# Kernel optimization log

Measured on AMD Instinct MI355X. Metric: run time of the kernel, lower is better.

Reference implementation:

```python
import jax, jax.numpy as jnp
import numpy as np

N_NODES = 50000
N_EDGES = 600000
D_IN = 128
D_HID = 128


def _sage_conv(x, src, dst, W_l, b_l, W_r):
    """PyG SAGEConv (mean aggr): out = lin_l(mean_{j in N(i)} x_j) + lin_r(x_i).
    bias lives in lin_l only."""
    n = x.shape[0]
    agg = jax.ops.segment_sum(x[src], dst, num_segments=n)            # [N, D]
    cnt = jax.ops.segment_sum(jnp.ones((src.shape[0],), x.dtype), dst, num_segments=n)
    mean = agg / jnp.maximum(cnt, 1.0)[:, None]
    return mean @ W_l.T + b_l + x @ W_r.T


def setup_inputs() -> dict:
    key = jax.random.key(0)
    ks = jax.random.split(key, 8)
    glorot = lambda k, o, i: jax.random.normal(k, (o, i), jnp.float32) * np.sqrt(2.0 / (o + i))
    return {
        "x": jax.random.normal(ks[0], (N_NODES, D_IN), jnp.float32),
        "edge_index": jax.random.randint(ks[1], (2, N_EDGES), 0, N_NODES, jnp.int64),
        "W1_l": glorot(ks[2], D_HID, D_IN),
        "b1": jnp.zeros((D_HID,), jnp.float32),
        "W1_r": glorot(ks[3], D_HID, D_IN),
        "W2_l": glorot(ks[4], D_HID, D_HID),
        "b2": jnp.zeros((D_HID,), jnp.float32),
        "W2_r": glorot(ks[5], D_HID, D_HID),
    }


def reference(x, edge_index, W1_l, b1, W1_r, W2_l, b2, W2_r):
    src, dst = edge_index[0], edge_index[1]
    h = _sage_conv(x, src, dst, W1_l, b1, W1_r)
    h = jax.nn.leaky_relu(h, negative_slope=0.2)
    return _sage_conv(h, src, dst, W2_l, b2, W2_r)
```

## Files before the change

kernel.cpp:

```cpp
#include <hip/hip_runtime.h>

#define N_NODES 50000
#define N_EDGES 600000
#define D 128
#define SCAN_BLOCKS ((N_NODES + 255) / 256)

typedef __attribute__((ext_vector_type(8))) short bf16x8;
typedef __attribute__((ext_vector_type(4))) float floatx4;

__device__ inline unsigned int f2bf(float f) {
    unsigned int u = __float_as_uint(f);
    return (u + 0x7FFFu + ((u >> 16) & 1u)) >> 16;
}
__device__ inline float bf_lo(unsigned int u) { return __uint_as_float(u << 16); }
__device__ inline float bf_hi(unsigned int u) { return __uint_as_float(u & 0xFFFF0000u); }

__global__ void k_prep(const float* __restrict__ x, unsigned short* __restrict__ xbf,
                       const float* __restrict__ wa, const float* __restrict__ wb,
                       const float* __restrict__ wc, const float* __restrict__ wd,
                       unsigned short* __restrict__ wbf,
                       const int* __restrict__ dst, int* __restrict__ cnt) {
    const int b = blockIdx.x;
    const int t = threadIdx.x;
    if (b < 6250) {
        int i = b * 256 + t;
        float4 v = ((const float4*)x)[i];
        uint2 o;
        o.x = f2bf(v.x) | (f2bf(v.y) << 16);
        o.y = f2bf(v.z) | (f2bf(v.w) << 16);
        ((uint2*)xbf)[i] = o;
    } else if (b < 6506) {
        int i = (b - 6250) * 256 + t;
        const float* srcs[4] = {wa, wb, wc, wd};
        wbf[i] = (unsigned short)f2bf(srcs[i >> 14][i & 16383]);
    } else {
        int e = (b - 6506) * 256 + t;
        if (e < N_EDGES) atomicAdd(&cnt[dst[e]], 1);
    }
}


__global__ void k_scan1(const int* __restrict__ cnt, int* __restrict__ off,
                        int* __restrict__ partial) {
    __shared__ int sdata[256];
    const int t = threadIdx.x;
    const int i = blockIdx.x * 256 + t;
    int v = (i < N_NODES) ? cnt[i] : 0;
    sdata[t] = v;
    __syncthreads();
    for (int d = 1; d < 256; d <<= 1) {
        int u = (t >= d) ? sdata[t - d] : 0;
        __syncthreads();
        sdata[t] += u;
        __syncthreads();
    }
    if (i < N_NODES) off[i] = sdata[t] - v;
    if (t == 255) partial[blockIdx.x] = sdata[255];
}

__global__ void k_scan2(int* __restrict__ partial) {
    __shared__ int sdata[256];
    const int t = threadIdx.x;
    int v = (t < SCAN_BLOCKS) ? partial[t] : 0;
    sdata[t] = v;
    __syncthreads();
    for (int d = 1; d < 256; d <<= 1) {
        int u = (t >= d) ? sdata[t - d] : 0;
        __syncthreads();
        sdata[t] += u;
        __syncthreads();
    }
    if (t < SCAN_BLOCKS) partial[t] = sdata[t] - v;
}

__global__ void k_scan3(int* __restrict__ off, const int* __restrict__ partial,
                        int* __restrict__ cursor) {
    const int i = blockIdx.x * 256 + threadIdx.x;
    if (i < N_NODES) {
        int o = off[i] + partial[blockIdx.x];
        off[i] = o;
        cursor[i] = o;
    }
    if (i == 0) off[N_NODES] = N_EDGES;
}

__global__ void k_bucket(const int* __restrict__ src, const int* __restrict__ dst,
                         int* __restrict__ cursor, int* __restrict__ ebuf) {
    int e = blockIdx.x * blockDim.x + threadIdx.x;
    if (e < N_EDGES) {
        int p = atomicAdd(&cursor[dst[e]], 1);
        ebuf[p] = src[e];
    }
}

template <bool RELU, bool OUT_BF16>
__global__ void __launch_bounds__(256) k_gather_layer(
    const int* __restrict__ off, const int* __restrict__ ebuf,
    const unsigned short* __restrict__ Xbf,
    const unsigned short* __restrict__ Wlbf, const float* __restrict__ bias,
    const unsigned short* __restrict__ Wrbf, void* __restrict__ outp) {
    __shared__ unsigned short tile[16][136];

    const int t = threadIdx.x;
    const int node0 = blockIdx.x * 16;

    {
        const int nl = t >> 4, q = t & 15;
        const int node = node0 + nl;
        int s0 = off[node], s1 = off[node + 1];
        float acc[8] = {0.f, 0.f, 0.f, 0.f, 0.f, 0.f, 0.f, 0.f};
        int e = s0;
        for (; e + 4 <= s1; e += 4) {
            int sa = ebuf[e], sb = ebuf[e + 1], sc = ebuf[e + 2], sd = ebuf[e + 3];
            uint4 va = *(const uint4*)(Xbf + (size_t)sa * D + q * 8);
            uint4 vb = *(const uint4*)(Xbf + (size_t)sb * D + q * 8);
            uint4 vc = *(const uint4*)(Xbf + (size_t)sc * D + q * 8);
            uint4 vd = *(const uint4*)(Xbf + (size_t)sd * D + q * 8);
            acc[0] += bf_lo(va.x) + bf_lo(vb.x) + bf_lo(vc.x) + bf_lo(vd.x);
            acc[1] += bf_hi(va.x) + bf_hi(vb.x) + bf_hi(vc.x) + bf_hi(vd.x);
            acc[2] += bf_lo(va.y) + bf_lo(vb.y) + bf_lo(vc.y) + bf_lo(vd.y);
            acc[3] += bf_hi(va.y) + bf_hi(vb.y) + bf_hi(vc.y) + bf_hi(vd.y);
            acc[4] += bf_lo(va.z) + bf_lo(vb.z) + bf_lo(vc.z) + bf_lo(vd.z);
            acc[5] += bf_hi(va.z) + bf_hi(vb.z) + bf_hi(vc.z) + bf_hi(vd.z);
            acc[6] += bf_lo(va.w) + bf_lo(vb.w) + bf_lo(vc.w) + bf_lo(vd.w);
            acc[7] += bf_hi(va.w) + bf_hi(vb.w) + bf_hi(vc.w) + bf_hi(vd.w);
        }
        for (; e < s1; ++e) {
            int sa = ebuf[e];
            uint4 va = *(const uint4*)(Xbf + (size_t)sa * D + q * 8);
            acc[0] += bf_lo(va.x); acc[1] += bf_hi(va.x);
            acc[2] += bf_lo(va.y); acc[3] += bf_hi(va.y);
            acc[4] += bf_lo(va.z); acc[5] += bf_hi(va.z);
            acc[6] += bf_lo(va.w); acc[7] += bf_hi(va.w);
        }
        float inv = (s1 > s0) ? 1.0f / (float)(s1 - s0) : 0.0f;
        uint4 o;
        o.x = f2bf(acc[0] * inv) | (f2bf(acc[1] * inv) << 16);
        o.y = f2bf(acc[2] * inv) | (f2bf(acc[3] * inv) << 16);
        o.z = f2bf(acc[4] * inv) | (f2bf(acc[5] * inv) << 16);
        o.w = f2bf(acc[6] * inv) | (f2bf(acc[7] * inv) << 16);
        *(uint4*)(&tile[nl][q * 8]) = o;
    }
    __syncthreads();

    const int lane = t & 63;
    const int wv = t >> 6;
    const int l15 = lane & 15;
    const int quad = lane >> 4;

    floatx4 c0 = (floatx4)(0.f), c1 = (floatx4)(0.f);
    const int nf0 = wv * 2, nf1 = wv * 2 + 1;

    const unsigned short* mrow = &tile[l15][quad * 8];
    const unsigned short* arowX = Xbf + (size_t)(node0 + l15) * D + quad * 8;

#pragma unroll
    for (int kk = 0; kk < 4; ++kk) {
        bf16x8 a = *(const bf16x8*)(mrow + kk * 32);
        bf16x8 b0 = *(const bf16x8*)(Wlbf + (size_t)(nf0 * 16 + l15) * D + kk * 32 + quad * 8);
        bf16x8 b1 = *(const bf16x8*)(Wlbf + (size_t)(nf1 * 16 + l15) * D + kk * 32 + quad * 8);
        c0 = __builtin_amdgcn_mfma_f32_16x16x32_bf16(a, b0, c0, 0, 0, 0);
        c1 = __builtin_amdgcn_mfma_f32_16x16x32_bf16(a, b1, c1, 0, 0, 0);
    }
#pragma unroll
    for (int kk = 0; kk < 4; ++kk) {
        bf16x8 a = *(const bf16x8*)(arowX + kk * 32);
        bf16x8 b0 = *(const bf16x8*)(Wrbf + (size_t)(nf0 * 16 + l15) * D + kk * 32 + quad * 8);
        bf16x8 b1 = *(const bf16x8*)(Wrbf + (size_t)(nf1 * 16 + l15) * D + kk * 32 + quad * 8);
        c0 = __builtin_amdgcn_mfma_f32_16x16x32_bf16(a, b0, c0, 0, 0, 0);
        c1 = __builtin_amdgcn_mfma_f32_16x16x32_bf16(a, b1, c1, 0, 0, 0);
    }

#pragma unroll
    for (int j = 0; j < 2; ++j) {
        floatx4 c = j ? c1 : c0;
        int f = (wv * 2 + j) * 16 + l15;
        float bv = bias[f];
#pragma unroll
        for (int r = 0; r < 4; ++r) {
            float v = c[r] + bv;
            if (RELU) v = v > 0.f ? v : 0.2f * v;
            int node = node0 + quad * 4 + r;
            if (OUT_BF16)
                ((unsigned short*)outp)[(size_t)node * D + f] = (unsigned short)f2bf(v);
            else
                ((float*)outp)[(size_t)node * D + f] = v;
        }
    }
}


extern "C" void kernel_launch(void* const* d_in, const int* in_sizes, int n_in,
                              void* d_out, int out_size, void* d_ws, size_t ws_size,
                              hipStream_t stream) {
    (void)in_sizes; (void)n_in; (void)out_size; (void)ws_size;

    const float* x   = (const float*)d_in[0];
    const int*   ei  = (const int*)d_in[1];
    const float* W1l = (const float*)d_in[2];
    const float* b1  = (const float*)d_in[3];
    const float* W1r = (const float*)d_in[4];
    const float* W2l = (const float*)d_in[5];
    const float* b2  = (const float*)d_in[6];
    const float* W2r = (const float*)d_in[7];

    const int* src = ei;
    const int* dst = ei + N_EDGES;

    char* ws = (char*)d_ws;
    int*   cnt     = (int*)(ws + 0);
    int*   off     = (int*)(ws + 200064);
    int*   cursor  = (int*)(ws + 400128);
    int*   partial = (int*)(ws + 600192);
    int*   ebuf    = (int*)(ws + 601216);
    unsigned short* wbf = (unsigned short*)(ws + 3001216);
    unsigned short* xbf = (unsigned short*)(ws + 3132288);
    unsigned short* hbf = (unsigned short*)(ws + 15932288);
    float* out = (float*)d_out;

    unsigned short* w1l_bf = wbf;
    unsigned short* w1r_bf = wbf + 16384;
    unsigned short* w2l_bf = wbf + 32768;
    unsigned short* w2r_bf = wbf + 49152;

    hipMemsetAsync(cnt, 0, N_NODES * sizeof(int), stream);
    k_prep<<<8850, 256, 0, stream>>>(x, xbf, W1l, W1r, W2l, W2r, wbf, dst, cnt);
    k_scan1<<<SCAN_BLOCKS, 256, 0, stream>>>(cnt, off, partial);
    k_scan2<<<1, 256, 0, stream>>>(partial);
    k_scan3<<<SCAN_BLOCKS, 256, 0, stream>>>(off, partial, cursor);
    k_bucket<<<(N_EDGES + 255) / 256, 256, 0, stream>>>(src, dst, cursor, ebuf);

    k_gather_layer<true, true><<<N_NODES / 16, 256, 0, stream>>>(
        off, ebuf, xbf, w1l_bf, b1, w1r_bf, (void*)hbf);
    k_gather_layer<false, false><<<N_NODES / 16, 256, 0, stream>>>(
        off, ebuf, hbf, w2l_bf, b2, w2r_bf, (void*)out);
}
```

Measured before the change: 251.8 us.

## Merge CSR build into one cooperative kernel and deepen gather unroll

Replaces the memset plus five preprocessing kernels (prep, three scan stages, bucket) with a single cooperative kernel of 512 blocks that uses grid-wide syncs between phases. The aim is to remove per-launch overhead and inter-kernel gaps. The partial-sum scan now covers 512 blocks, with each thread of block 0 handling two entries. Separately, the neighbor gather loop gains an 8-wide unrolled stage that issues eight row loads before accumulating, to expose more memory-level parallelism. The risk is that grid.sync cost and reduced parallelism (512 blocks doing grid-stride loops over x conversion and edges) may offset the launch savings.

```diff
diff --git a/kernel.cpp b/kernel.cpp
--- a/kernel.cpp
+++ b/kernel.cpp
@@ -1,9 +1,13 @@
 #include <hip/hip_runtime.h>
+#include <hip/hip_cooperative_groups.h>
+
+namespace cg = cooperative_groups;
 
 #define N_NODES 50000
 #define N_EDGES 600000
 #define D 128
-#define SCAN_BLOCKS ((N_NODES + 255) / 256)
+#define BUILD_BLOCKS 512
+#define BUILD_THREADS (BUILD_BLOCKS * 256)
 
 typedef __attribute__((ext_vector_type(8))) short bf16x8;
 typedef __attribute__((ext_vector_type(4))) float floatx4;
@@ -15,37 +19,38 @@
 __device__ inline float bf_lo(unsigned int u) { return __uint_as_float(u << 16); }
 __device__ inline float bf_hi(unsigned int u) { return __uint_as_float(u & 0xFFFF0000u); }
 
-__global__ void k_prep(const float* __restrict__ x, unsigned short* __restrict__ xbf,
-                       const float* __restrict__ wa, const float* __restrict__ wb,
-                       const float* __restrict__ wc, const float* __restrict__ wd,
-                       unsigned short* __restrict__ wbf,
-                       const int* __restrict__ dst, int* __restrict__ cnt) {
+__global__ void __launch_bounds__(256) k_build(
+    const float* __restrict__ x, unsigned short* __restrict__ xbf,
+    const float* __restrict__ wa, const float* __restrict__ wb,
+    const float* __restrict__ wc, const float* __restrict__ wd,
+    unsigned short* __restrict__ wbf,
+    const int* __restrict__ src, const int* __restrict__ dst,
+    int* __restrict__ cnt, int* __restrict__ off, int* __restrict__ cursor,
+    int* __restrict__ partial, int* __restrict__ ebuf) {
+    cg::grid_group grid = cg::this_grid();
+    __shared__ int sdata[256];
+    const int t = threadIdx.x;
     const int b = blockIdx.x;
-    const int t = threadIdx.x;
-    if (b < 6250) {
-        int i = b * 256 + t;
+    const int gtid = b * 256 + t;
+
+    for (int i = gtid; i < N_NODES; i += BUILD_THREADS) cnt[i] = 0;
+    for (int i = gtid; i < N_NODES * D / 4; i += BUILD_THREADS) {
         float4 v = ((const float4*)x)[i];
         uint2 o;
         o.x = f2bf(v.x) | (f2bf(v.y) << 16);
         o.y = f2bf(v.z) | (f2bf(v.w) << 16);
         ((uint2*)xbf)[i] = o;
-    } else if (b < 6506) {
-        int i = (b - 6250) * 256 + t;
+    }
+    if (gtid < 65536) {
         const float* srcs[4] = {wa, wb, wc, wd};
-        wbf[i] = (unsigned short)f2bf(srcs[i >> 14][i & 16383]);
-    } else {
-        int e = (b - 6506) * 256 + t;
-        if (e < N_EDGES) atomicAdd(&cnt[dst[e]], 1);
-    }
-}
-
-
-__global__ void k_scan1(const int* __restrict__ cnt, int* __restrict__ off,
-                        int* __restrict__ partial) {
-    __shared__ int sdata[256];
-    const int t = threadIdx.x;
-    const int i = blockIdx.x * 256 + t;
-    int v = (i < N_NODES) ? cnt[i] : 0;
+        wbf[gtid] = (unsigned short)f2bf(srcs[gtid >> 14][gtid & 16383]);
+    }
+    grid.sync();
+
+    for (int e = gtid; e < N_EDGES; e += BUILD_THREADS) atomicAdd(&cnt[dst[e]], 1);
+    grid.sync();
+
+    int v = (gtid < N_NODES) ? cnt[gtid] : 0;
     sdata[t] = v;
     __syncthreads();
     for (int d = 1; d < 256; d <<= 1) {
@@ -54,40 +59,36 @@
         sdata[t] += u;
         __syncthreads();
     }
-    if (i < N_NODES) off[i] = sdata[t] - v;
-    if (t == 255) partial[blockIdx.x] = sdata[255];
-}
-
-__global__ void k_scan2(int* __restrict__ partial) {
-    __shared__ int sdata[256];
-    const int t = threadIdx.x;
-    int v = (t < SCAN_BLOCKS) ? partial[t] : 0;
-    sdata[t] = v;
-    __syncthreads();
-    for (int d = 1; d < 256; d <<= 1) {
-        int u = (t >= d) ? sdata[t - d] : 0;
+    if (gtid < N_NODES) off[gtid] = sdata[t] - v;
+    if (t == 255) partial[b] = sdata[255];
+    grid.sync();
+
+    if (b == 0) {
+        int p0 = partial[2 * t], p1 = partial[2 * t + 1];
+        int pr = p0 + p1;
+        sdata[t] = pr;
         __syncthreads();
-        sdata[t] += u;
-        __syncthreads();
-    }
-    if (t < SCAN_BLOCKS) partial[t] = sdata[t] - v;
-}
-
-__global__ void k_scan3(int* __restrict__ off, const int* __restrict__ partial,
-                        int* __restrict__ cursor) {
-    const int i = blockIdx.x * 256 + threadIdx.x;
-    if (i < N_NODES) {
-        int o = off[i] + partial[blockIdx.x];
-        off[i] = o;
-        cursor[i] = o;
-    }
-    if (i == 0) off[N_NODES] = N_EDGES;
-}
-
-__global__ void k_bucket(const int* __restrict__ src, const int* __restrict__ dst,
-                         int* __restrict__ cursor, int* __restrict__ ebuf) {
-    int e = blockIdx.x * blockDim.x + threadIdx.x;
-    if (e < N_EDGES) {
+        for (int d = 1; d < 256; d <<= 1) {
+            int u = (t >= d) ? sdata[t - d] : 0;
+            __syncthreads();
+            sdata[t] += u;
+            __syncthreads();
+        }
+        int excl = sdata[t] - pr;
+        partial[2 * t] = excl;
+        partial[2 * t + 1] = excl + p0;
+    }
+    grid.sync();
+
+    if (gtid < N_NODES) {
+        int o = off[gtid] + partial[b];
+        off[gtid] = o;
+        cursor[gtid] = o;
+    }
+    if (gtid == 0) off[N_NODES] = N_EDGES;
+    grid.sync();
+
+    for (int e = gtid; e < N_EDGES; e += BUILD_THREADS) {
         int p = atomicAdd(&cursor[dst[e]], 1);
         ebuf[p] = src[e];
     }
@@ -110,24 +111,34 @@
         int s0 = off[node], s1 = off[node + 1];
         float acc[8] = {0.f, 0.f, 0.f, 0.f, 0.f, 0.f, 0.f, 0.f};
         int e = s0;
+        for (; e + 8 <= s1; e += 8) {
+            uint4 w[8];
+#pragma unroll
+            for (int j = 0; j < 8; ++j)
+                w[j] = *(const uint4*)(Xbf + (size_t)ebuf[e + j] * D + q * 8);
+#pragma unroll
+            for (int j = 0; j < 8; ++j) {
+                acc[0] += bf_lo(w[j].x); acc[1] += bf_hi(w[j].x);
+                acc[2] += bf_lo(w[j].y); acc[3] += bf_hi(w[j].y);
+                acc[4] += bf_lo(w[j].z); acc[5] += bf_hi(w[j].z);
+                acc[6] += bf_lo(w[j].w); acc[7] += bf_hi(w[j].w);
+            }
+        }
         for (; e + 4 <= s1; e += 4) {
-            int sa = ebuf[e], sb = ebuf[e + 1], sc = ebuf[e + 2], sd = ebuf[e + 3];
-            uint4 va = *(const uint4*)(Xbf + (size_t)sa * D + q * 8);
-            uint4 vb = *(const uint4*)(Xbf + (size_t)sb * D + q * 8);
-            uint4 vc = *(const uint4*)(Xbf + (size_t)sc * D + q * 8);
-            uint4 vd = *(const uint4*)(Xbf + (size_t)sd * D + q * 8);
-            acc[0] += bf_lo(va.x) + bf_lo(vb.x) + bf_lo(vc.x) + bf_lo(vd.x);
-            acc[1] += bf_hi(va.x) + bf_hi(vb.x) + bf_hi(vc.x) + bf_hi(vd.x);
-            acc[2] += bf_lo(va.y) + bf_lo(vb.y) + bf_lo(vc.y) + bf_lo(vd.y);
-            acc[3] += bf_hi(va.y) + bf_hi(vb.y) + bf_hi(vc.y) + bf_hi(vd.y);
-            acc[4] += bf_lo(va.z) + bf_lo(vb.z) + bf_lo(vc.z) + bf_lo(vd.z);
-            acc[5] += bf_hi(va.z) + bf_hi(vb.z) + bf_hi(vc.z) + bf_hi(vd.z);
-            acc[6] += bf_lo(va.w) + bf_lo(vb.w) + bf_lo(vc.w) + bf_lo(vd.w);
-            acc[7] += bf_hi(va.w) + bf_hi(vb.w) + bf_hi(vc.w) + bf_hi(vd.w);
+            uint4 w[4];
+#pragma unroll
+            for (int j = 0; j < 4; ++j)
+                w[j] = *(const uint4*)(Xbf + (size_t)ebuf[e + j] * D + q * 8);
+#pragma unroll
+            for (int j = 0; j < 4; ++j) {
+                acc[0] += bf_lo(w[j].x); acc[1] += bf_hi(w[j].x);
+                acc[2] += bf_lo(w[j].y); acc[3] += bf_hi(w[j].y);
+                acc[4] += bf_lo(w[j].z); acc[5] += bf_hi(w[j].z);
+                acc[6] += bf_lo(w[j].w); acc[7] += bf_hi(w[j].w);
+            }
         }
         for (; e < s1; ++e) {
-            int sa = ebuf[e];
-            uint4 va = *(const uint4*)(Xbf + (size_t)sa * D + q * 8);
+            uint4 va = *(const uint4*)(Xbf + (size_t)ebuf[e] * D + q * 8);
             acc[0] += bf_lo(va.x); acc[1] += bf_hi(va.x);
             acc[2] += bf_lo(va.y); acc[3] += bf_hi(va.y);
             acc[4] += bf_lo(va.z); acc[5] += bf_hi(va.z);
@@ -212,10 +223,10 @@
     int*   off     = (int*)(ws + 200064);
     int*   cursor  = (int*)(ws + 400128);
     int*   partial = (int*)(ws + 600192);
-    int*   ebuf    = (int*)(ws + 601216);
-    unsigned short* wbf = (unsigned short*)(ws + 3001216);
-    unsigned short* xbf = (unsigned short*)(ws + 3132288);
-    unsigned short* hbf = (unsigned short*)(ws + 15932288);
+    int*   ebuf    = (int*)(ws + 602240);
+    unsigned short* wbf = (unsigned short*)(ws + 3002240);
+    unsigned short* xbf = (unsigned short*)(ws + 3133312);
+    unsigned short* hbf = (unsigned short*)(ws + 15933312);
     float* out = (float*)d_out;
 
     unsigned short* w1l_bf = wbf;
@@ -223,12 +234,14 @@
     unsigned short* w2l_bf = wbf + 32768;
     unsigned short* w2r_bf = wbf + 49152;
 
-    hipMemsetAsync(cnt, 0, N_NODES * sizeof(int), stream);
-    k_prep<<<8850, 256, 0, stream>>>(x, xbf, W1l, W1r, W2l, W2r, wbf, dst, cnt);
-    k_scan1<<<SCAN_BLOCKS, 256, 0, stream>>>(cnt, off, partial);
-    k_scan2<<<1, 256, 0, stream>>>(partial);
-    k_scan3<<<SCAN_BLOCKS, 256, 0, stream>>>(off, partial, cursor);
-    k_bucket<<<(N_EDGES + 255) / 256, 256, 0, stream>>>(src, dst, cursor, ebuf);
+    void* args[] = {
+        (void*)&x, (void*)&xbf,
+        (void*)&W1l, (void*)&W1r, (void*)&W2l, (void*)&W2r, (void*)&wbf,
+        (void*)&src, (void*)&dst,
+        (void*)&cnt, (void*)&off, (void*)&cursor, (void*)&partial, (void*)&ebuf
+    };
+    hipLaunchCooperativeKernel((void*)k_build, dim3(BUILD_BLOCKS), dim3(256),
+                               args, 0, stream);
 
     k_gather_layer<true, true><<<N_NODES / 16, 256, 0, stream>>>(
         off, ebuf, xbf, w1l_bf, b1, w1r_bf, (void*)hbf);
```

New measurement: 548.5 us. +117.8%, slower.

## Balance neighbor gather across block threads using LDS atomic accumulation

Applied to the files above, without the earlier changes.

Replaces the per-node gather, where each group of 16 threads walked one node's edge list, with a flat loop over all edges of the block's 16 nodes. Each edge is found by binary search in shared offsets and added into a shared float accumulator with LDS atomics. This targets load imbalance and idle threads caused by uneven node degrees. In exchange it issues eight LDS atomic adds per element and makes summation order nondeterministic.

```diff
diff --git a/kernel.cpp b/kernel.cpp
--- a/kernel.cpp
+++ b/kernel.cpp
@@ -99,46 +99,53 @@
     const unsigned short* __restrict__ Xbf,
     const unsigned short* __restrict__ Wlbf, const float* __restrict__ bias,
     const unsigned short* __restrict__ Wrbf, void* __restrict__ outp) {
+    __shared__ int s_off[17];
+    __shared__ float accf[16][132];
     __shared__ unsigned short tile[16][136];
 
     const int t = threadIdx.x;
     const int node0 = blockIdx.x * 16;
+
+    if (t < 17) s_off[t] = off[node0 + t];
+    for (int i = t; i < 16 * 132; i += 256) ((float*)accf)[i] = 0.f;
+    __syncthreads();
+
+    {
+        const int e0 = s_off[0];
+        const int items = (s_off[16] - e0) * 16;
+        const int q = t & 15;
+#pragma unroll 2
+        for (int it = t; it < items; it += 256) {
+            int eidx = e0 + (it >> 4);
+            int s = ebuf[eidx];
+            uint4 v = *(const uint4*)(Xbf + (size_t)s * D + q * 8);
+            int nl = 0;
+#pragma unroll
+            for (int step = 8; step >= 1; step >>= 1)
+                if (s_off[nl + step] <= eidx) nl += step;
+            float* arow = &accf[nl][q * 8];
+            atomicAdd(arow + 0, bf_lo(v.x));
+            atomicAdd(arow + 1, bf_hi(v.x));
+            atomicAdd(arow + 2, bf_lo(v.y));
+            atomicAdd(arow + 3, bf_hi(v.y));
+            atomicAdd(arow + 4, bf_lo(v.z));
+            atomicAdd(arow + 5, bf_hi(v.z));
+            atomicAdd(arow + 6, bf_lo(v.w));
+            atomicAdd(arow + 7, bf_hi(v.w));
+        }
+    }
+    __syncthreads();
 
     {
         const int nl = t >> 4, q = t & 15;
-        const int node = node0 + nl;
-        int s0 = off[node], s1 = off[node + 1];
-        float acc[8] = {0.f, 0.f, 0.f, 0.f, 0.f, 0.f, 0.f, 0.f};
-        int e = s0;
-        for (; e + 4 <= s1; e += 4) {
-            int sa = ebuf[e], sb = ebuf[e + 1], sc = ebuf[e + 2], sd = ebuf[e + 3];
-            uint4 va = *(const uint4*)(Xbf + (size_t)sa * D + q * 8);
-            uint4 vb = *(const uint4*)(Xbf + (size_t)sb * D + q * 8);
-            uint4 vc = *(const uint4*)(Xbf + (size_t)sc * D + q * 8);
-            uint4 vd = *(const uint4*)(Xbf + (size_t)sd * D + q * 8);
-            acc[0] += bf_lo(va.x) + bf_lo(vb.x) + bf_lo(vc.x) + bf_lo(vd.x);
-            acc[1] += bf_hi(va.x) + bf_hi(vb.x) + bf_hi(vc.x) + bf_hi(vd.x);
-            acc[2] += bf_lo(va.y) + bf_lo(vb.y) + bf_lo(vc.y) + bf_lo(vd.y);
-            acc[3] += bf_hi(va.y) + bf_hi(vb.y) + bf_hi(vc.y) + bf_hi(vd.y);
-            acc[4] += bf_lo(va.z) + bf_lo(vb.z) + bf_lo(vc.z) + bf_lo(vd.z);
-            acc[5] += bf_hi(va.z) + bf_hi(vb.z) + bf_hi(vc.z) + bf_hi(vd.z);
-            acc[6] += bf_lo(va.w) + bf_lo(vb.w) + bf_lo(vc.w) + bf_lo(vd.w);
-            acc[7] += bf_hi(va.w) + bf_hi(vb.w) + bf_hi(vc.w) + bf_hi(vd.w);
-        }
-        for (; e < s1; ++e) {
-            int sa = ebuf[e];
-            uint4 va = *(const uint4*)(Xbf + (size_t)sa * D + q * 8);
-            acc[0] += bf_lo(va.x); acc[1] += bf_hi(va.x);
-            acc[2] += bf_lo(va.y); acc[3] += bf_hi(va.y);
-            acc[4] += bf_lo(va.z); acc[5] += bf_hi(va.z);
-            acc[6] += bf_lo(va.w); acc[7] += bf_hi(va.w);
-        }
-        float inv = (s1 > s0) ? 1.0f / (float)(s1 - s0) : 0.0f;
+        int deg = s_off[nl + 1] - s_off[nl];
+        float inv = (deg > 0) ? 1.0f / (float)deg : 0.0f;
+        const float* a = &accf[nl][q * 8];
         uint4 o;
-        o.x = f2bf(acc[0] * inv) | (f2bf(acc[1] * inv) << 16);
-        o.y = f2bf(acc[2] * inv) | (f2bf(acc[3] * inv) << 16);
-        o.z = f2bf(acc[4] * inv) | (f2bf(acc[5] * inv) << 16);
-        o.w = f2bf(acc[6] * inv) | (f2bf(acc[7] * inv) << 16);
+        o.x = f2bf(a[0] * inv) | (f2bf(a[1] * inv) << 16);
+        o.y = f2bf(a[2] * inv) | (f2bf(a[3] * inv) << 16);
+        o.z = f2bf(a[4] * inv) | (f2bf(a[5] * inv) << 16);
+        o.w = f2bf(a[6] * inv) | (f2bf(a[7] * inv) << 16);
         *(uint4*)(&tile[nl][q * 8]) = o;
     }
     __syncthreads();
```

Measured after the change: 997.9 us. 3.96x slower.
